# Optimization experiments

Hardware: AMD Instinct MI355X
Metric: run time of the kernel (lower is better)

## Reference

```python
import jax, jax.numpy as jnp
import numpy as np
import math
from jax import lax

B, C, L = 16, 512, 1024
NCONV, K, H = 4, 7, 8
DH = C // H


def setup_inputs() -> dict:
    key = jax.random.key(0)
    ks = jax.random.split(key, 8)
    s = 0.02
    return {
        "inputx": jax.random.normal(ks[0], (B, C, L), jnp.float32),
        "mask": jnp.ones((B, L), jnp.int32),
        "number_of_layers": 1,
        "blocks": 1,
        "norm_c_scale": jnp.ones((NCONV, C), jnp.float32),
        "norm_c_bias": jnp.zeros((NCONV, C), jnp.float32),
        "dw_w": jax.random.normal(ks[1], (NCONV, C, K), jnp.float32) * s,
        "pw_w": jax.random.normal(ks[2], (NCONV, C, C), jnp.float32) * s,
        "pw_b": jnp.zeros((NCONV, C), jnp.float32),
        "ln1_s": jnp.ones((C,), jnp.float32),
        "ln1_b": jnp.zeros((C,), jnp.float32),
        "ln2_s": jnp.ones((C,), jnp.float32),
        "ln2_b": jnp.zeros((C,), jnp.float32),
        "w_kv": jax.random.normal(ks[3], (2 * C, C), jnp.float32) * s,
        "w_q": jax.random.normal(ks[4], (C, C), jnp.float32) * s,
        "ffn1_w": jax.random.normal(ks[5], (C, C), jnp.float32) * s,
        "ffn1_b": jnp.zeros((C,), jnp.float32),
        "ffn2_w": jax.random.normal(ks[6], (C, C), jnp.float32) * s,
        "ffn2_b": jnp.zeros((C,), jnp.float32),
    }


def _ln(x, s, b, eps=1e-5):  # x: [B, L, C], normalize over C
    mu = jnp.mean(x, axis=-1, keepdims=True)
    var = jnp.mean((x - mu) ** 2, axis=-1, keepdims=True)
    return (x - mu) * lax.rsqrt(var + eps) * s + b


def _ln_ch(x, s, b):  # x: [B, C, L] -> LayerNorm over channel dim
    return _ln(x.transpose(0, 2, 1), s, b).transpose(0, 2, 1)


def _pos_enc(x, minimum=1.0, maximum=10000.0):  # x: [B, C, L]
    xt = x.transpose(0, 2, 1)  # [B, L, C]
    ns = C // 2
    log_inc = math.log(maximum / minimum) / (ns - 1)
    inv = minimum * jnp.exp(jnp.arange(ns, dtype=jnp.float32) * -log_inc)
    pos = jnp.arange(L, dtype=jnp.float32)
    scaled = pos[:, None] * inv[None, :]  # [L, ns]
    sig = jnp.concatenate([jnp.sin(scaled), jnp.cos(scaled)], axis=1)  # [L, 2*ns]
    if C % 2 == 1:
        sig = jnp.pad(sig, ((0, 0), (0, 1)))
    return (xt + sig[None]).transpose(0, 2, 1)


def _conv1x1(w, x, b=None):  # w: [O, I], x: [B, I, L]
    y = jnp.einsum('oi,bil->bol', w, x)
    if b is not None:
        y = y + b[:, None]
    return y


def _dwconv(x, w):  # x: [B, C, L], w: [C, K], groups=C, same padding
    return lax.conv_general_dilated(
        x, w[:, None, :], window_strides=(1,), padding=[(K // 2, K // 2)],
        feature_group_count=C, dimension_numbers=('NCH', 'OIH', 'NCH'))


def _attention(x, mask, w_kv, w_q):  # x: [B, C, L]
    kv = _conv1x1(w_kv, x).transpose(0, 2, 1)  # [B, L, 2C]
    q = _conv1x1(w_q, x).transpose(0, 2, 1)    # [B, L, C]
    k, v = kv[..., :C], kv[..., C:]

    def split(t):  # [B, L, C] -> [B, H, L, DH]
        return t.reshape(B, L, H, DH).transpose(0, 2, 1, 3)

    q, k, v = split(q) * (DH ** -0.5), split(k), split(v)
    logits = jnp.einsum('bhqd,bhkd->bhqk', q, k)
    maskf = mask[:, None, None, :].astype(jnp.float32)
    logits = logits + (-1e30) * (1.0 - maskf)
    w = jax.nn.softmax(logits, axis=-1)
    o = jnp.einsum('bhqk,bhkd->bhqd', w, v)
    return o.transpose(0, 2, 1, 3).reshape(B, L, C).transpose(0, 2, 1)


def reference(inputx, mask, number_of_layers, blocks, norm_c_scale, norm_c_bias,
              dw_w, pw_w, pw_b, ln1_s, ln1_b, ln2_s, ln2_b, w_kv, w_q,
              ffn1_w, ffn1_b, ffn2_w, ffn2_b):
    # Eval-mode forward: dropout and stochastic depth are identity.
    result = _pos_enc(inputx)
    for i in range(NCONV):
        res = result
        h = _ln_ch(result, norm_c_scale[i], norm_c_bias[i])
        h = _dwconv(h, dw_w[i])
        h = jax.nn.relu(_conv1x1(pw_w[i], h, pw_b[i]))
        result = h + res
    res = result
    h = _ln_ch(result, ln1_s, ln1_b)
    result = _attention(h, mask, w_kv, w_q) + res
    res = result
    h = _ln_ch(result, ln2_s, ln2_b)
    h = jax.nn.relu(_conv1x1(ffn1_w, h, ffn1_b))
    h = _conv1x1(ffn2_w, h, ffn2_b)
    return h + res
```

## Files before the change

kernel.cpp:

```cpp
#include <hip/hip_runtime.h>
#include <math.h>

#define BB 16
#define CC 512
#define LL 1024
#define NCONV 4
#define KW 7
#define NH 8
#define DH 64

typedef short short8 __attribute__((ext_vector_type(8)));
typedef float f32x4  __attribute__((ext_vector_type(4)));

union bfpack2 { __bf16 h[2]; unsigned u; };
union bfpack4 { __bf16 h[4]; uint2 v; };
union bfpack8 { __bf16 h[8]; uint4 v; };

__device__ __forceinline__ void gload_lds16(const void* g, void* l) {
    __builtin_amdgcn_global_load_lds(
        (const __attribute__((address_space(1))) void*)g,
        (__attribute__((address_space(3))) void*)l, 16, 0, 0);
}

__global__ __launch_bounds__(256) void wprep_kernel(
    const float* __restrict__ pw, const float* __restrict__ wkv,
    const float* __restrict__ wq, const float* __restrict__ f1,
    const float* __restrict__ f2, __bf16* __restrict__ out)
{
    const int S = CC * CC;
    int i = (blockIdx.x * 256 + threadIdx.x) * 4;
    const float* src; int base;
    if (i < 4 * S)      { src = pw;  base = 0; }
    else if (i < 6 * S) { src = wkv; base = 4 * S; }
    else if (i < 7 * S) { src = wq;  base = 6 * S; }
    else if (i < 8 * S) { src = f1;  base = 7 * S; }
    else                { src = f2;  base = 8 * S; }
    float4 f = *(const float4*)(src + (i - base));
    bfpack4 p;
    p.h[0] = (__bf16)f.x; p.h[1] = (__bf16)f.y;
    p.h[2] = (__bf16)f.z; p.h[3] = (__bf16)f.w;
    *(uint2*)(out + i) = p.v;
}

__global__ __launch_bounds__(256) void dw_transpose_kernel(
    const float* __restrict__ w, __bf16* __restrict__ wt)
{
    int t = blockIdx.x * 256 + threadIdx.x;
    if (t < NCONV * KW * CC) {
        int c = t & (CC - 1);
        int k = (t >> 9) % KW;
        int i = t / (KW * CC);
        wt[t] = (__bf16)w[(i * CC + c) * KW + k];
    }
}

__global__ __launch_bounds__(256) void pos_enc_t_kernel(
    const float* __restrict__ x, float* __restrict__ out)
{
    __shared__ float T[64 * 65];
    const int b = blockIdx.z, c0 = blockIdx.y * 64, l0 = blockIdx.x * 64;
    const int t = threadIdx.x;
    {
        int lt = t & 63, cr0 = t >> 6;
        #pragma unroll
        for (int j = 0; j < 16; ++j) {
            int cr = cr0 + 4 * j;
            T[cr * 65 + lt] = x[((size_t)b * CC + c0 + cr) * LL + l0 + lt];
        }
    }
    __syncthreads();
    {
        int ct = t & 63, lr0 = t >> 6;
        const float log_inc = 0.03611898185f;
        int c = c0 + ct;
        int half = (c < CC / 2) ? c : c - CC / 2;
        float inv = __expf(-log_inc * (float)half);
        #pragma unroll
        for (int j = 0; j < 16; ++j) {
            int lr = lr0 + 4 * j;
            int l = l0 + lr;
            float ph = (float)l * inv;
            float sig = (c < CC / 2) ? __sinf(ph) : __cosf(ph);
            out[((size_t)b * LL + l) * CC + c] = T[ct * 65 + lr] + sig;
        }
    }
}

__global__ __launch_bounds__(256) void ln_last_kernel(
    const float* __restrict__ x, const float* __restrict__ gam,
    const float* __restrict__ bet, __bf16* __restrict__ out)
{
    int row = blockIdx.x * 4 + (threadIdx.x >> 6);
    int ln = threadIdx.x & 63;
    const float* xr = x + (size_t)row * CC + ln * 8;
    float4 a = *(const float4*)xr;
    float4 c = *(const float4*)(xr + 4);
    float sum = a.x + a.y + a.z + a.w + c.x + c.y + c.z + c.w;
    float sq  = a.x*a.x + a.y*a.y + a.z*a.z + a.w*a.w
              + c.x*c.x + c.y*c.y + c.z*c.z + c.w*c.w;
    #pragma unroll
    for (int off = 1; off < 64; off <<= 1) {
        sum += __shfl_xor(sum, off);
        sq  += __shfl_xor(sq, off);
    }
    float mean = sum * (1.0f / CC);
    float rstd = rsqrtf(sq * (1.0f / CC) - mean * mean + 1e-5f);
    float4 g0 = *(const float4*)(gam + ln * 8);
    float4 g1 = *(const float4*)(gam + ln * 8 + 4);
    float4 b0 = *(const float4*)(bet + ln * 8);
    float4 b1 = *(const float4*)(bet + ln * 8 + 4);
    bfpack8 p;
    p.h[0] = (__bf16)((a.x - mean) * rstd * g0.x + b0.x);
    p.h[1] = (__bf16)((a.y - mean) * rstd * g0.y + b0.y);
    p.h[2] = (__bf16)((a.z - mean) * rstd * g0.z + b0.z);
    p.h[3] = (__bf16)((a.w - mean) * rstd * g0.w + b0.w);
    p.h[4] = (__bf16)((c.x - mean) * rstd * g1.x + b1.x);
    p.h[5] = (__bf16)((c.y - mean) * rstd * g1.y + b1.y);
    p.h[6] = (__bf16)((c.z - mean) * rstd * g1.z + b1.z);
    p.h[7] = (__bf16)((c.w - mean) * rstd * g1.w + b1.w);
    *(uint4*)(out + (size_t)row * CC + ln * 8) = p.v;
}

__global__ __launch_bounds__(256) void ln_dw_kernel(
    const float* __restrict__ x, const float* __restrict__ gam,
    const float* __restrict__ bet, const __bf16* __restrict__ wt,
    __bf16* __restrict__ out)
{
    __shared__ __attribute__((aligned(16))) __bf16 Hs[40][CC];
    const int b = blockIdx.y;
    const int l0 = blockIdx.x * 32;
    const int t = threadIdx.x;
    const int w = t >> 6, ln = t & 63;

    float4 g0 = *(const float4*)(gam + ln * 8);
    float4 g1 = *(const float4*)(gam + ln * 8 + 4);
    float4 bb0 = *(const float4*)(bet + ln * 8);
    float4 bb1 = *(const float4*)(bet + ln * 8 + 4);

    #pragma unroll
    for (int p = 0; p < 10; ++p) {
        int ri = p * 4 + w;
        int l = l0 - 4 + ri;
        if (l < 0 || l >= LL) {
            uint4 z = {0u, 0u, 0u, 0u};
            *(uint4*)(&Hs[ri][ln * 8]) = z;
        } else {
            const float* xr = x + ((size_t)b * LL + l) * CC + ln * 8;
            float4 a = *(const float4*)xr;
            float4 c = *(const float4*)(xr + 4);
            float sum = a.x + a.y + a.z + a.w + c.x + c.y + c.z + c.w;
            float sq  = a.x*a.x + a.y*a.y + a.z*a.z + a.w*a.w
                      + c.x*c.x + c.y*c.y + c.z*c.z + c.w*c.w;
            #pragma unroll
            for (int off = 1; off < 64; off <<= 1) {
                sum += __shfl_xor(sum, off);
                sq  += __shfl_xor(sq, off);
            }
            float mean = sum * (1.0f / CC);
            float rstd = rsqrtf(sq * (1.0f / CC) - mean * mean + 1e-5f);
            bfpack8 pp;
            pp.h[0] = (__bf16)((a.x - mean) * rstd * g0.x + bb0.x);
            pp.h[1] = (__bf16)((a.y - mean) * rstd * g0.y + bb0.y);
            pp.h[2] = (__bf16)((a.z - mean) * rstd * g0.z + bb0.z);
            pp.h[3] = (__bf16)((a.w - mean) * rstd * g0.w + bb0.w);
            pp.h[4] = (__bf16)((c.x - mean) * rstd * g1.x + bb1.x);
            pp.h[5] = (__bf16)((c.y - mean) * rstd * g1.y + bb1.y);
            pp.h[6] = (__bf16)((c.z - mean) * rstd * g1.z + bb1.z);
            pp.h[7] = (__bf16)((c.w - mean) * rstd * g1.w + bb1.w);
            *(uint4*)(&Hs[ri][ln * 8]) = pp.v;
        }
    }
    __syncthreads();

    const int cc0 = (t & 63) * 8;
    bfpack8 wv[KW];
    #pragma unroll
    for (int k = 0; k < KW; ++k) wv[k].v = *(const uint4*)(wt + k * CC + cc0);
    #pragma unroll
    for (int j = 0; j < 8; ++j) {
        int r = (t >> 6) + 4 * j;
        float acc[8] = {};
        #pragma unroll
        for (int k = 0; k < KW; ++k) {
            bfpack8 xv;
            xv.v = *(const uint4*)(&Hs[r + 1 + k][cc0]);
            #pragma unroll
            for (int i2 = 0; i2 < 8; ++i2)
                acc[i2] += (float)xv.h[i2] * (float)wv[k].h[i2];
        }
        bfpack8 o;
        #pragma unroll
        for (int i2 = 0; i2 < 8; ++i2) o.h[i2] = (__bf16)acc[i2];
        *(uint4*)(out + ((size_t)b * LL + l0 + r) * CC + cc0) = o.v;
    }
}

__global__ __launch_bounds__(256) void gemm_bf_kernel(
    const __bf16* __restrict__ Wm, const __bf16* __restrict__ X,
    void* __restrict__ Yv, const float* __restrict__ bias,
    const float* __restrict__ res, const int mode, const int relu,
    const float scale)
{
    const int b  = blockIdx.z;
    const int l0 = blockIdx.x * 128;
    const int o0 = blockIdx.y * 128;
    const __bf16* Xb = X + (size_t)b * LL * CC;

    __shared__ __attribute__((aligned(16))) __bf16 Al0[128 * 64];
    __shared__ __attribute__((aligned(16))) __bf16 Al1[128 * 64];
    __shared__ __attribute__((aligned(16))) __bf16 Bl0[128 * 64];
    __shared__ __attribute__((aligned(16))) __bf16 Bl1[128 * 64];

    const int tid = threadIdx.x;
    const int wave = tid >> 6, lane = tid & 63;
    const int wm = wave >> 1, wn = wave & 1;
    const int ln = lane & 15, kq = lane >> 4;

    const int swapped = (mode >= 2);
    const __bf16* Aptr = swapped ? (Xb + (size_t)l0 * CC) : (Wm + (size_t)o0 * CC);
    const __bf16* Bptr = swapped ? (Wm + (size_t)o0 * CC) : (Xb + (size_t)l0 * CC);

    f32x4 acc[4][4] = {};

    const int srow  = tid >> 3;
    const int sc    = ((tid & 7) ^ (srow & 7)) * 8;
    const int lbase = wave * 8 * 64;

    auto STAGE = [&](__bf16* Ad, __bf16* Bd, int k0) {
        #pragma unroll
        for (int j = 0; j < 4; ++j) {
            gload_lds16(Aptr + (size_t)(j * 32 + srow) * CC + k0 + sc,
                        Ad + j * 32 * 64 + lbase);
            gload_lds16(Bptr + (size_t)(j * 32 + srow) * CC + k0 + sc,
                        Bd + j * 32 * 64 + lbase);
        }
    };
    auto COMPUTE = [&](const __bf16* As, const __bf16* Bs) {
        #pragma unroll
        for (int kk = 0; kk < 2; ++kk) {
            const int so = ((kk * 4 + kq) ^ (ln & 7)) * 8;
            short8 af[4], bfr[4];
            #pragma unroll
            for (int mi = 0; mi < 4; ++mi)
                af[mi] = *(const short8*)(As + (wm * 64 + mi * 16 + ln) * 64 + so);
            #pragma unroll
            for (int ni = 0; ni < 4; ++ni)
                bfr[ni] = *(const short8*)(Bs + (wn * 64 + ni * 16 + ln) * 64 + so);
            #pragma unroll
            for (int mi = 0; mi < 4; ++mi)
                #pragma unroll
                for (int ni = 0; ni < 4; ++ni)
                    acc[mi][ni] = __builtin_amdgcn_mfma_f32_16x16x32_bf16(
                        af[mi], bfr[ni], acc[mi][ni], 0, 0, 0);
        }
    };

    STAGE(Al0, Bl0, 0);
    __syncthreads();
    #pragma unroll
    for (int k0 = 0; k0 < CC; k0 += 128) {
        STAGE(Al1, Bl1, k0 + 64);
        COMPUTE(Al0, Bl0);
        __syncthreads();
        if (k0 + 128 < CC) {
            STAGE(Al0, Bl0, k0 + 128);
            COMPUTE(Al1, Bl1);
            __syncthreads();
        } else {
            COMPUTE(Al1, Bl1);
        }
    }

    if (mode == 0) {
        float* Y = (float*)Yv;
        #pragma unroll
        for (int mi = 0; mi < 4; ++mi) {
            int cb = o0 + wm * 64 + mi * 16 + kq * 4;
            #pragma unroll
            for (int ni = 0; ni < 4; ++ni) {
                int l = l0 + wn * 64 + ni * 16 + ln;
                size_t idx = ((size_t)b * LL + l) * CC + cb;
                float4 r4 = *(const float4*)(Y + idx);
                float4 v;
                v.x = fmaxf(acc[mi][ni][0] + bias[cb + 0], 0.f) + r4.x;
                v.y = fmaxf(acc[mi][ni][1] + bias[cb + 1], 0.f) + r4.y;
                v.z = fmaxf(acc[mi][ni][2] + bias[cb + 2], 0.f) + r4.z;
                v.w = fmaxf(acc[mi][ni][3] + bias[cb + 3], 0.f) + r4.w;
                *(float4*)(Y + idx) = v;
            }
        }
    } else if (mode == 1) {
        __bf16* Y = (__bf16*)Yv;
        #pragma unroll
        for (int mi = 0; mi < 4; ++mi) {
            int cb = o0 + wm * 64 + mi * 16 + kq * 4;
            #pragma unroll
            for (int ni = 0; ni < 4; ++ni) {
                int l = l0 + wn * 64 + ni * 16 + ln;
                bfpack4 p;
                #pragma unroll
                for (int i = 0; i < 4; ++i) {
                    float v = acc[mi][ni][i] * scale;
                    if (bias) v += bias[cb + i];
                    if (relu) v = fmaxf(v, 0.f);
                    p.h[i] = (__bf16)v;
                }
                *(uint2*)(Y + ((size_t)b * LL + l) * CC + cb) = p.v;
            }
        }
    } else {
        float* Y = (float*)Yv;
        #pragma unroll
        for (int mi = 0; mi < 4; ++mi) {
            int lb = l0 + wm * 64 + mi * 16 + kq * 4;
            #pragma unroll
            for (int ni = 0; ni < 4; ++ni) {
                int c = o0 + wn * 64 + ni * 16 + ln;
                float bv = bias[c];
                const float* rp = res + ((size_t)b * LL + lb) * CC + c;
                float4 v;
                v.x = acc[mi][ni][0] + bv + rp[0 * CC];
                v.y = acc[mi][ni][1] + bv + rp[1 * CC];
                v.z = acc[mi][ni][2] + bv + rp[2 * CC];
                v.w = acc[mi][ni][3] + bv + rp[3 * CC];
                *(float4*)(Y + ((size_t)b * CC + c) * LL + lb) = v;
            }
        }
    }
}

__global__ __launch_bounds__(256) void qkv_gemm_kernel(
    const __bf16* __restrict__ wkv, const __bf16* __restrict__ wq,
    const __bf16* __restrict__ X, __bf16* __restrict__ kout,
    __bf16* __restrict__ vout, __bf16* __restrict__ qout)
{
    const int b  = blockIdx.z;
    const int l0 = blockIdx.x * 128;
    const int sel = blockIdx.y >> 2;
    const int o0 = (blockIdx.y & 3) * 128;
    const __bf16* Xb = X + (size_t)b * LL * CC;
    const __bf16* Wsel = (sel == 0) ? wkv : (sel == 1 ? wkv + CC * CC : wq);

    __shared__ __attribute__((aligned(16))) __bf16 Al[128 * 32];
    __shared__ __attribute__((aligned(16))) __bf16 Bl[128 * 32];

    const int tid = threadIdx.x;
    const int wave = tid >> 6, lane = tid & 63;
    const int wm = wave >> 1, wn = wave & 1;
    const int ln = lane & 15, kq = lane >> 4;

    const int swapped = (sel == 1);
    const __bf16* Aptr = swapped ? (Xb + (size_t)l0 * CC) : (Wsel + (size_t)o0 * CC);
    const __bf16* Bptr = swapped ? (Wsel + (size_t)o0 * CC) : (Xb + (size_t)l0 * CC);

    f32x4 acc[4][4] = {};

    const int r0 = tid >> 2;
    const int ce = (tid & 3) * 8;
    __bf16* lA0 = Al + wave * 512;
    __bf16* lA1 = Al + 2048 + wave * 512;
    __bf16* lB0 = Bl + wave * 512;
    __bf16* lB1 = Bl + 2048 + wave * 512;

    for (int k0 = 0; k0 < CC; k0 += 32) {
        __syncthreads();
        gload_lds16(Aptr + (size_t)r0 * CC + k0 + ce, lA0);
        gload_lds16(Aptr + (size_t)(r0 + 64) * CC + k0 + ce, lA1);
        gload_lds16(Bptr + (size_t)r0 * CC + k0 + ce, lB0);
        gload_lds16(Bptr + (size_t)(r0 + 64) * CC + k0 + ce, lB1);
        __syncthreads();

        short8 af[4], bfr[4];
        #pragma unroll
        for (int mi = 0; mi < 4; ++mi)
            af[mi] = *(const short8*)(Al + (wm * 64 + mi * 16 + ln) * 32 + kq * 8);
        #pragma unroll
        for (int ni = 0; ni < 4; ++ni)
            bfr[ni] = *(const short8*)(Bl + (wn * 64 + ni * 16 + ln) * 32 + kq * 8);
        #pragma unroll
        for (int mi = 0; mi < 4; ++mi)
            #pragma unroll
            for (int ni = 0; ni < 4; ++ni)
                acc[mi][ni] = __builtin_amdgcn_mfma_f32_16x16x32_bf16(
                    af[mi], bfr[ni], acc[mi][ni], 0, 0, 0);
    }

    if (sel == 1) {
        #pragma unroll
        for (int mi = 0; mi < 4; ++mi) {
            int lb = l0 + wm * 64 + mi * 16 + kq * 4;
            #pragma unroll
            for (int ni = 0; ni < 4; ++ni) {
                int c = o0 + wn * 64 + ni * 16 + ln;
                bfpack4 p;
                #pragma unroll
                for (int i = 0; i < 4; ++i) p.h[i] = (__bf16)acc[mi][ni][i];
                *(uint2*)(vout + ((size_t)b * CC + c) * LL + lb) = p.v;
            }
        }
    } else {
        __bf16* Y = (sel == 0) ? kout : qout;
        const float scale = (sel == 0) ? 1.0f : 0.18033688011f;
        #pragma unroll
        for (int mi = 0; mi < 4; ++mi) {
            int cb = o0 + wm * 64 + mi * 16 + kq * 4;
            #pragma unroll
            for (int ni = 0; ni < 4; ++ni) {
                int l = l0 + wn * 64 + ni * 16 + ln;
                bfpack4 p;
                #pragma unroll
                for (int i = 0; i < 4; ++i)
                    p.h[i] = (__bf16)(acc[mi][ni][i] * scale);
                *(uint2*)(Y + ((size_t)b * LL + l) * CC + cb) = p.v;
            }
        }
    }
}

__global__ __launch_bounds__(256) void attn_mfma_kernel(
    const __bf16* __restrict__ qb, const __bf16* __restrict__ kb,
    const __bf16* __restrict__ vb, const int* __restrict__ maskp,
    float* __restrict__ outp)
{
    const int b = blockIdx.z, hh = blockIdx.y, ql0 = blockIdx.x * 64;
    const int tid = threadIdx.x, w = tid >> 6, lane = tid & 63;
    const int ln = lane & 15, kq = lane >> 4;

    __shared__ __bf16 Kl[64 * 72];
    __shared__ __bf16 Vl[64 * 72];
    __shared__ __bf16 Pl[64 * 72];

    const int co = hh * 64;
    const int sr = tid >> 3, sc8 = (tid & 7) * 8;

    short8 qf[2];
    #pragma unroll
    for (int c = 0; c < 2; ++c)
        qf[c] = *(const short8*)(qb + ((size_t)b * LL + ql0 + w * 16 + ln) * CC
                                 + co + c * 32 + kq * 8);

    float l_run = 0.f;
    f32x4 oacc[4] = {};

    uint4 kv0, kv1, vv0, vv1;
    kv0 = *(const uint4*)(kb + ((size_t)b * LL + sr) * CC + co + sc8);
    kv1 = *(const uint4*)(kb + ((size_t)b * LL + sr + 32) * CC + co + sc8);
    vv0 = *(const uint4*)(vb + ((size_t)(b * CC + co + sr)) * LL + sc8);
    vv1 = *(const uint4*)(vb + ((size_t)(b * CC + co + sr + 32)) * LL + sc8);

    for (int m0 = 0; m0 < LL; m0 += 64) {
        __syncthreads();
        *(uint4*)(Kl + sr * 72 + sc8)        = kv0;
        *(uint4*)(Kl + (sr + 32) * 72 + sc8) = kv1;
        *(uint4*)(Vl + sr * 72 + sc8)        = vv0;
        *(uint4*)(Vl + (sr + 32) * 72 + sc8) = vv1;
        __syncthreads();
        {
            int mn = (m0 + 64 < LL) ? m0 + 64 : m0;
            kv0 = *(const uint4*)(kb + ((size_t)b * LL + mn + sr) * CC + co + sc8);
            kv1 = *(const uint4*)(kb + ((size_t)b * LL + mn + sr + 32) * CC + co + sc8);
            vv0 = *(const uint4*)(vb + ((size_t)(b * CC + co + sr)) * LL + mn + sc8);
            vv1 = *(const uint4*)(vb + ((size_t)(b * CC + co + sr + 32)) * LL + mn + sc8);
        }

        f32x4 s[4] = {};
        __builtin_amdgcn_s_setprio(1);
        #pragma unroll
        for (int ni = 0; ni < 4; ++ni)
            #pragma unroll
            for (int c = 0; c < 2; ++c) {
                short8 bk = *(const short8*)(Kl + (ni * 16 + ln) * 72 + c * 32 + kq * 8);
                s[ni] = __builtin_amdgcn_mfma_f32_16x16x32_bf16(bk, qf[c], s[ni], 0, 0, 0);
            }
        __builtin_amdgcn_s_setprio(0);

        #pragma unroll
        for (int ni = 0; ni < 4; ++ni) {
            int4 mv = *(const int4*)(maskp + b * LL + m0 + ni * 16 + kq * 4);
            float p0 = exp2f(mv.x ? s[ni][0] : -1e30f);
            float p1 = exp2f(mv.y ? s[ni][1] : -1e30f);
            float p2 = exp2f(mv.z ? s[ni][2] : -1e30f);
            float p3 = exp2f(mv.w ? s[ni][3] : -1e30f);
            l_run += (p0 + p1) + (p2 + p3);
            bfpack4 p4;
            p4.h[0] = (__bf16)p0; p4.h[1] = (__bf16)p1;
            p4.h[2] = (__bf16)p2; p4.h[3] = (__bf16)p3;
            *(uint2*)(Pl + (w * 16 + ln) * 72 + ni * 16 + kq * 4) = p4.v;
        }
        asm volatile("s_waitcnt lgkmcnt(0)" ::: "memory");

        short8 bp[2];
        #pragma unroll
        for (int c = 0; c < 2; ++c)
            bp[c] = *(const short8*)(Pl + (w * 16 + ln) * 72 + c * 32 + kq * 8);
        __builtin_amdgcn_s_setprio(1);
        #pragma unroll
        for (int ni = 0; ni < 4; ++ni)
            #pragma unroll
            for (int c = 0; c < 2; ++c) {
                short8 av = *(const short8*)(Vl + (ni * 16 + ln) * 72 + c * 32 + kq * 8);
                oacc[ni] = __builtin_amdgcn_mfma_f32_16x16x32_bf16(av, bp[c], oacc[ni], 0, 0, 0);
            }
        __builtin_amdgcn_s_setprio(0);
    }

    l_run += __shfl_xor(l_run, 16);
    l_run += __shfl_xor(l_run, 32);
    float inv = 1.0f / l_run;

    int l = ql0 + w * 16 + ln;
    #pragma unroll
    for (int ni = 0; ni < 4; ++ni) {
        int c = co + ni * 16 + kq * 4;
        size_t idx = ((size_t)b * LL + l) * CC + c;
        float4 r4 = *(const float4*)(outp + idx);
        r4.x += oacc[ni][0] * inv;
        r4.y += oacc[ni][1] * inv;
        r4.z += oacc[ni][2] * inv;
        r4.w += oacc[ni][3] * inv;
        *(float4*)(outp + idx) = r4;
    }
}

extern "C" void kernel_launch(void* const* d_in, const int* in_sizes, int n_in,
                              void* d_out, int out_size, void* d_ws, size_t ws_size,
                              hipStream_t stream)
{
    const float* inputx  = (const float*)d_in[0];
    const int*   mask    = (const int*)  d_in[1];
    const float* ncs     = (const float*)d_in[4];
    const float* ncb     = (const float*)d_in[5];
    const float* dw_w    = (const float*)d_in[6];
    const float* pw_w    = (const float*)d_in[7];
    const float* pw_b    = (const float*)d_in[8];
    const float* ln1_s   = (const float*)d_in[9];
    const float* ln1_b   = (const float*)d_in[10];
    const float* ln2_s   = (const float*)d_in[11];
    const float* ln2_b   = (const float*)d_in[12];
    const float* w_kv    = (const float*)d_in[13];
    const float* w_q     = (const float*)d_in[14];
    const float* ffn1_w  = (const float*)d_in[15];
    const float* ffn1_b  = (const float*)d_in[16];
    const float* ffn2_w  = (const float*)d_in[17];
    const float* ffn2_b  = (const float*)d_in[18];

    const size_t NT = (size_t)BB * CC * LL;
    float*  result = (float*)d_ws;
    __bf16* wsb  = (__bf16*)(result + NT);
    __bf16* hb   = wsb;
    __bf16* xb   = wsb + NT;
    __bf16* qbuf = wsb + 2 * NT;
    __bf16* kbuf = wsb + 3 * NT;
    __bf16* vbuf = wsb + 4 * NT;
    __bf16* wpw  = wsb + 5 * NT;
    __bf16* wkv  = wpw + 4 * CC * CC;
    __bf16* wq   = wkv + 2 * CC * CC;
    __bf16* wf1  = wq + CC * CC;
    __bf16* wf2  = wf1 + CC * CC;
    __bf16* dwt  = wf2 + CC * CC;

    dim3 blk(256);
    dim3 ggrid(LL / 128, CC / 128, BB);

    wprep_kernel<<<9 * CC * CC / 1024, blk, 0, stream>>>(pw_w, w_kv, w_q, ffn1_w, ffn2_w, wpw);
    dw_transpose_kernel<<<(NCONV * KW * CC + 255) / 256, blk, 0, stream>>>(dw_w, dwt);

    pos_enc_t_kernel<<<dim3(LL / 64, CC / 64, BB), blk, 0, stream>>>(inputx, result);

    for (int i = 0; i < NCONV; ++i) {
        ln_dw_kernel<<<dim3(LL / 32, BB), blk, 0, stream>>>(
            result, ncs + i * CC, ncb + i * CC, dwt + i * KW * CC, xb);
        gemm_bf_kernel<<<ggrid, blk, 0, stream>>>(wpw + (size_t)i * CC * CC, xb, result,
                                                  pw_b + i * CC, nullptr, 0, 1, 1.0f);
    }

    ln_last_kernel<<<BB * LL / 4, blk, 0, stream>>>(result, ln1_s, ln1_b, hb);
    qkv_gemm_kernel<<<dim3(LL / 128, 12, BB), blk, 0, stream>>>(wkv, wq, hb, kbuf, vbuf, qbuf);
    attn_mfma_kernel<<<dim3(LL / 64, NH, BB), blk, 0, stream>>>(qbuf, kbuf, vbuf, mask, result);

    ln_last_kernel<<<BB * LL / 4, blk, 0, stream>>>(result, ln2_s, ln2_b, hb);
    gemm_bf_kernel<<<ggrid, blk, 0, stream>>>(wf1, hb, xb, ffn1_b, nullptr, 1, 1, 1.0f);
    gemm_bf_kernel<<<ggrid, blk, 0, stream>>>(wf2, xb, d_out, ffn2_b, result, 2, 0, 1.0f);
}
```

Baseline: 440.1 us.

## Double-buffer LDS with async global-to-LDS loads and XOR swizzle in QKV and attention

The QKV GEMM now stages 64-wide K tiles into two LDS buffers with direct global-to-LDS loads, so the next tile loads while the current one is computed and barriers drop to one per 64-wide K step. The attention kernel replaces register-staged, padded K/V tiles with ping-pong LDS buffers filled by global_load_lds. All LDS layouts use an XOR swizzle instead of padding to avoid bank conflicts. This costs more LDS per block, which may lower occupancy, and the swizzle index math must match on every read and write.

```diff
diff --git a/kernel.cpp b/kernel.cpp
--- a/kernel.cpp
+++ b/kernel.cpp
@@ -341,8 +341,10 @@
     const __bf16* Xb = X + (size_t)b * LL * CC;
     const __bf16* Wsel = (sel == 0) ? wkv : (sel == 1 ? wkv + CC * CC : wq);
 
-    __shared__ __attribute__((aligned(16))) __bf16 Al[128 * 32];
-    __shared__ __attribute__((aligned(16))) __bf16 Bl[128 * 32];
+    __shared__ __attribute__((aligned(16))) __bf16 Al0[128 * 64];
+    __shared__ __attribute__((aligned(16))) __bf16 Al1[128 * 64];
+    __shared__ __attribute__((aligned(16))) __bf16 Bl0[128 * 64];
+    __shared__ __attribute__((aligned(16))) __bf16 Bl1[128 * 64];
 
     const int tid = threadIdx.x;
     const int wave = tid >> 6, lane = tid & 63;
@@ -355,34 +357,53 @@
 
     f32x4 acc[4][4] = {};
 
-    const int r0 = tid >> 2;
-    const int ce = (tid & 3) * 8;
-    __bf16* lA0 = Al + wave * 512;
-    __bf16* lA1 = Al + 2048 + wave * 512;
-    __bf16* lB0 = Bl + wave * 512;
-    __bf16* lB1 = Bl + 2048 + wave * 512;
-
-    for (int k0 = 0; k0 < CC; k0 += 32) {
+    const int srow  = tid >> 3;
+    const int sc    = ((tid & 7) ^ (srow & 7)) * 8;
+    const int lbase = wave * 8 * 64;
+
+    auto STAGE = [&](__bf16* Ad, __bf16* Bd, int k0) {
+        #pragma unroll
+        for (int j = 0; j < 4; ++j) {
+            gload_lds16(Aptr + (size_t)(j * 32 + srow) * CC + k0 + sc,
+                        Ad + j * 32 * 64 + lbase);
+            gload_lds16(Bptr + (size_t)(j * 32 + srow) * CC + k0 + sc,
+                        Bd + j * 32 * 64 + lbase);
+        }
+    };
+    auto COMPUTE = [&](const __bf16* As, const __bf16* Bs) {
+        #pragma unroll
+        for (int kk = 0; kk < 2; ++kk) {
+            const int so = ((kk * 4 + kq) ^ (ln & 7)) * 8;
+            short8 af[4], bfr[4];
+            #pragma unroll
+            for (int mi = 0; mi < 4; ++mi)
+                af[mi] = *(const short8*)(As + (wm * 64 + mi * 16 + ln) * 64 + so);
+            #pragma unroll
+            for (int ni = 0; ni < 4; ++ni)
+                bfr[ni] = *(const short8*)(Bs + (wn * 64 + ni * 16 + ln) * 64 + so);
+            #pragma unroll
+            for (int mi = 0; mi < 4; ++mi)
+                #pragma unroll
+                for (int ni = 0; ni < 4; ++ni)
+                    acc[mi][ni] = __builtin_amdgcn_mfma_f32_16x16x32_bf16(
+                        af[mi], bfr[ni], acc[mi][ni], 0, 0, 0);
+        }
+    };
+
+    STAGE(Al0, Bl0, 0);
+    __syncthreads();
+    #pragma unroll
+    for (int k0 = 0; k0 < CC; k0 += 128) {
+        STAGE(Al1, Bl1, k0 + 64);
+        COMPUTE(Al0, Bl0);
         __syncthreads();
-        gload_lds16(Aptr + (size_t)r0 * CC + k0 + ce, lA0);
-        gload_lds16(Aptr + (size_t)(r0 + 64) * CC + k0 + ce, lA1);
-        gload_lds16(Bptr + (size_t)r0 * CC + k0 + ce, lB0);
-        gload_lds16(Bptr + (size_t)(r0 + 64) * CC + k0 + ce, lB1);
-        __syncthreads();
-
-        short8 af[4], bfr[4];
-        #pragma unroll
-        for (int mi = 0; mi < 4; ++mi)
-            af[mi] = *(const short8*)(Al + (wm * 64 + mi * 16 + ln) * 32 + kq * 8);
-        #pragma unroll
-        for (int ni = 0; ni < 4; ++ni)
-            bfr[ni] = *(const short8*)(Bl + (wn * 64 + ni * 16 + ln) * 32 + kq * 8);
-        #pragma unroll
-        for (int mi = 0; mi < 4; ++mi)
-            #pragma unroll
-            for (int ni = 0; ni < 4; ++ni)
-                acc[mi][ni] = __builtin_amdgcn_mfma_f32_16x16x32_bf16(
-                    af[mi], bfr[ni], acc[mi][ni], 0, 0, 0);
+        if (k0 + 128 < CC) {
+            STAGE(Al0, Bl0, k0 + 128);
+            COMPUTE(Al1, Bl1);
+            __syncthreads();
+        } else {
+            COMPUTE(Al1, Bl1);
+        }
     }
 
     if (sel == 1) {
@@ -426,12 +447,14 @@
     const int tid = threadIdx.x, w = tid >> 6, lane = tid & 63;
     const int ln = lane & 15, kq = lane >> 4;
 
-    __shared__ __bf16 Kl[64 * 72];
-    __shared__ __bf16 Vl[64 * 72];
-    __shared__ __bf16 Pl[64 * 72];
+    __shared__ __attribute__((aligned(16))) __bf16 K0l[64 * 64];
+    __shared__ __attribute__((aligned(16))) __bf16 K1l[64 * 64];
+    __shared__ __attribute__((aligned(16))) __bf16 V0l[64 * 64];
+    __shared__ __attribute__((aligned(16))) __bf16 V1l[64 * 64];
+    __shared__ __attribute__((aligned(16))) __bf16 Pl [64 * 64];
 
     const int co = hh * 64;
-    const int sr = tid >> 3, sc8 = (tid & 7) * 8;
+    const int srow = tid >> 3, slot = tid & 7;
 
     short8 qf[2];
     #pragma unroll
@@ -442,34 +465,27 @@
     float l_run = 0.f;
     f32x4 oacc[4] = {};
 
-    uint4 kv0, kv1, vv0, vv1;
-    kv0 = *(const uint4*)(kb + ((size_t)b * LL + sr) * CC + co + sc8);
-    kv1 = *(const uint4*)(kb + ((size_t)b * LL + sr + 32) * CC + co + sc8);
-    vv0 = *(const uint4*)(vb + ((size_t)(b * CC + co + sr)) * LL + sc8);
-    vv1 = *(const uint4*)(vb + ((size_t)(b * CC + co + sr + 32)) * LL + sc8);
-
-    for (int m0 = 0; m0 < LL; m0 += 64) {
-        __syncthreads();
-        *(uint4*)(Kl + sr * 72 + sc8)        = kv0;
-        *(uint4*)(Kl + (sr + 32) * 72 + sc8) = kv1;
-        *(uint4*)(Vl + sr * 72 + sc8)        = vv0;
-        *(uint4*)(Vl + (sr + 32) * 72 + sc8) = vv1;
-        __syncthreads();
-        {
-            int mn = (m0 + 64 < LL) ? m0 + 64 : m0;
-            kv0 = *(const uint4*)(kb + ((size_t)b * LL + mn + sr) * CC + co + sc8);
-            kv1 = *(const uint4*)(kb + ((size_t)b * LL + mn + sr + 32) * CC + co + sc8);
-            vv0 = *(const uint4*)(vb + ((size_t)(b * CC + co + sr)) * LL + mn + sc8);
-            vv1 = *(const uint4*)(vb + ((size_t)(b * CC + co + sr + 32)) * LL + mn + sc8);
-        }
-
+    auto STAGE = [&](__bf16* Kd, __bf16* Vd, int m0) {
+        #pragma unroll
+        for (int j = 0; j < 2; ++j) {
+            int row = srow + 32 * j;
+            int gs = (slot ^ (row & 7)) * 8;
+            gload_lds16(kb + ((size_t)b * LL + m0 + row) * CC + co + gs,
+                        Kd + j * 2048 + w * 512);
+            gload_lds16(vb + ((size_t)(b * CC + co + row)) * LL + m0 + gs,
+                        Vd + j * 2048 + w * 512);
+        }
+    };
+
+    auto TILE = [&](const __bf16* Kc, const __bf16* Vc, int m0) {
         f32x4 s[4] = {};
         __builtin_amdgcn_s_setprio(1);
         #pragma unroll
         for (int ni = 0; ni < 4; ++ni)
             #pragma unroll
             for (int c = 0; c < 2; ++c) {
-                short8 bk = *(const short8*)(Kl + (ni * 16 + ln) * 72 + c * 32 + kq * 8);
+                short8 bk = *(const short8*)(Kc + (ni * 16 + ln) * 64
+                                             + (((c * 4 + kq) ^ (ln & 7)) * 8));
                 s[ni] = __builtin_amdgcn_mfma_f32_16x16x32_bf16(bk, qf[c], s[ni], 0, 0, 0);
             }
         __builtin_amdgcn_s_setprio(0);
@@ -485,23 +501,36 @@
             bfpack4 p4;
             p4.h[0] = (__bf16)p0; p4.h[1] = (__bf16)p1;
             p4.h[2] = (__bf16)p2; p4.h[3] = (__bf16)p3;
-            *(uint2*)(Pl + (w * 16 + ln) * 72 + ni * 16 + kq * 4) = p4.v;
+            int s16 = (2 * ni + (kq >> 1)) ^ (ln & 7);
+            *(uint2*)(Pl + (w * 16 + ln) * 64 + s16 * 8 + (kq & 1) * 4) = p4.v;
         }
         asm volatile("s_waitcnt lgkmcnt(0)" ::: "memory");
 
         short8 bp[2];
         #pragma unroll
         for (int c = 0; c < 2; ++c)
-            bp[c] = *(const short8*)(Pl + (w * 16 + ln) * 72 + c * 32 + kq * 8);
+            bp[c] = *(const short8*)(Pl + (w * 16 + ln) * 64
+                                     + (((c * 4 + kq) ^ (ln & 7)) * 8));
         __builtin_amdgcn_s_setprio(1);
         #pragma unroll
         for (int ni = 0; ni < 4; ++ni)
             #pragma unroll
             for (int c = 0; c < 2; ++c) {
-                short8 av = *(const short8*)(Vl + (ni * 16 + ln) * 72 + c * 32 + kq * 8);
+                short8 av = *(const short8*)(Vc + (ni * 16 + ln) * 64
+                                             + (((c * 4 + kq) ^ (ln & 7)) * 8));
                 oacc[ni] = __builtin_amdgcn_mfma_f32_16x16x32_bf16(av, bp[c], oacc[ni], 0, 0, 0);
             }
         __builtin_amdgcn_s_setprio(0);
+    };
+
+    STAGE(K0l, V0l, 0);
+    for (int m0 = 0; m0 < LL; m0 += 128) {
+        __syncthreads();
+        if (m0 + 64 < LL) STAGE(K1l, V1l, m0 + 64);
+        TILE(K0l, V0l, m0);
+        __syncthreads();
+        if (m0 + 128 < LL) STAGE(K0l, V0l, m0 + 128);
+        TILE(K1l, V1l, m0 + 64);
     }
 
     l_run += __shfl_xor(l_run, 16);
```

Measured after the change: 439.8 us. About the same (-0.1%).
